# Kernel optimization log

Measured on AMD Instinct MI355X. Metric: run time of the kernel, lower is better.

Reference implementation:

```python
import jax, jax.numpy as jnp
import numpy as np

B, TQ, TK, D, R, H = 4, 2048, 2048, 1024, 64, 512
TAU_BASE, ASTRO_DECAY = 1.0, 0.95


def setup_inputs() -> dict:
    key = jax.random.key(0)
    ks = jax.random.split(key, 20)
    xav = lambda k, din, dout: jax.random.uniform(k, (din, dout), jnp.float32, -1.0, 1.0) * np.sqrt(6.0 / (din + dout))
    inp = {
        'q_in': jax.random.normal(ks[0], (B, TQ, D), jnp.float32),
        'k_in': jax.random.normal(ks[1], (B, TK, D), jnp.float32),
        'v_in': jax.random.normal(ks[2], (B, TK, D), jnp.float32),
        'astrocyte_state': jnp.zeros((B,), jnp.float32),
        'Wq': xav(ks[3], D, D), 'bq': jnp.zeros((D,), jnp.float32),
        'Wk': xav(ks[4], D, D), 'bk': jnp.zeros((D,), jnp.float32),
        'Wv': xav(ks[5], D, D), 'bv': jnp.zeros((D,), jnp.float32),
        'Wo': xav(ks[6], D, D), 'bo': jnp.zeros((D,), jnp.float32),
        # orthonormal role rows (R <= D): QR of a random D x R matrix, rows = Q^T
        'role_matrix': jnp.linalg.qr(jax.random.normal(ks[7], (D, R), jnp.float32))[0].T,
        'Wr1': xav(ks[8], D, H), 'br1': jnp.zeros((H,), jnp.float32),
        'Wr2': xav(ks[9], H, R),
        'astro_scale': jnp.ones((1,), jnp.float32),
    }
    return inp


def _l2norm(x, axis=-1, eps=1e-12):
    return x / jnp.clip(jnp.linalg.norm(x, axis=axis, keepdims=True), eps)


def _bind_vectors(a, b):
    # holographic (circular-convolution) binding via FFT along feature dim
    n = a.shape[-1]
    return jnp.fft.irfft(jnp.fft.rfft(a, axis=-1) * jnp.fft.rfft(b, axis=-1), n=n, axis=-1)


def _compute_surprise(Q):
    # per-token surprise: RMS-normalized L2 magnitude of projected queries -> (B, T_q)
    return jnp.linalg.norm(Q, axis=-1) / np.sqrt(Q.shape[-1])


def reference(q_in, k_in, v_in, astrocyte_state, Wq, bq, Wk, bk, Wv, bv, Wo, bo,
              role_matrix, Wr1, br1, Wr2, astro_scale):
    Q = q_in @ Wq + bq                      # (B,TQ,D)
    K = k_in @ Wk + bk                      # (B,TK,D)
    V = v_in @ Wv + bv                      # (B,TK,D)

    role_mat_norm = _l2norm(role_matrix)    # (R,D)
    role_logits = jax.nn.relu(K @ Wr1 + br1) @ Wr2          # (B,TK,R)
    role_weights = jax.nn.softmax(role_logits, axis=-1)
    role_vecs = role_weights @ role_mat_norm                 # (B,TK,D)
    K_bound = _bind_vectors(K, role_vecs)                    # (B,TK,D)

    surprise = _compute_surprise(Q)                          # (B,TQ)
    mean_surprise = surprise.mean(axis=-1)                   # (B,)
    new_state = ASTRO_DECAY * astrocyte_state + (1.0 - ASTRO_DECAY) * mean_surprise
    tau_eff = TAU_BASE * jnp.clip(1.0 + astro_scale * new_state, 0.001)[:, None, None]

    q_n = _l2norm(Q)
    k_n = _l2norm(K_bound)
    cos_sim = jnp.einsum('bqd,bkd->bqk', q_n, k_n)           # (B,TQ,TK)
    x = (cos_sim + 1.0) * 0.5
    scores = jnp.clip(1.0 - tau_eff * (1.0 - x) ** 2, 0.0)   # Epanechnikov kernel
    attn = scores / jnp.clip(scores.sum(axis=-1, keepdims=True), 1e-9)
    context = jnp.einsum('bqk,bkd->bqd', attn, V)
    output = context @ Wo + bo
    return output, new_state
```

## Files before the change

### kernel.cpp

```cpp
#include <hip/hip_runtime.h>
#include <stdint.h>


#define Bq 4
#define Tq 2048
#define Dd 1024
#define NT 8192
#define Hh 512
#define Rr_ 64
#define FQ 1024

typedef unsigned short ushort_t;
typedef short s16x8 __attribute__((ext_vector_type(8)));
typedef float floatx4 __attribute__((ext_vector_type(4)));

__device__ __forceinline__ float b2f(ushort_t s) {
  unsigned u = (unsigned)s << 16;
  return __builtin_bit_cast(float, u);
}
__device__ __forceinline__ ushort_t f2b(float f) {
  unsigned u = __builtin_bit_cast(unsigned, f);
  unsigned r = (u + 0x7fffu + ((u >> 16) & 1u)) >> 16;
  return (ushort_t)r;
}

__device__ __forceinline__ void load_lds16(const void* g, void* l) {
  __builtin_amdgcn_global_load_lds((__attribute__((address_space(1))) void*)(g),
                                   (__attribute__((address_space(3))) void*)(l),
                                   16, 0, 0);
}

__global__ __launch_bounds__(256) void gemm_bt(
    const ushort_t* __restrict__ A, const ushort_t* __restrict__ Bt,
    float* __restrict__ C, ushort_t* __restrict__ Cbf,
    const float* __restrict__ bias_col, const float* __restrict__ bias_row,
    const float* __restrict__ rmul, int rmulStride,
    const float* __restrict__ cmul, int cmulStride,
    const float* __restrict__ tau,
    float* __restrict__ rowsum, int rsStride, int rsMode,
    int K, int lda, int ldb, int ldc,
    long long sA, long long sB, long long sC, int flags)
{
  __shared__ __align__(16) ushort_t As[128 * 32];
  __shared__ __align__(16) ushort_t Bs[128 * 32];

  const int bz   = blockIdx.z;
  const ushort_t* Ab = A + (size_t)bz * sA;
  const ushort_t* Bb = Bt + (size_t)bz * sB;
  const int tm   = blockIdx.y * 128;
  const int tn   = blockIdx.x * 128;
  const int tid  = threadIdx.x;
  const int wave = tid >> 6;
  const int lane = tid & 63;
  const int wm   = (wave & 1) << 6;
  const int wn   = (wave >> 1) << 6;
  const int sr   = lane >> 2;
  const int cp   = lane & 3;
  const int sc   = (((cp - (sr >> 1)) & 3) << 3);
  const int fr   = lane & 15;
  const int fk   = ((((lane >> 4) + (fr >> 1)) & 3) << 3);

  floatx4 acc[4][4] = {};

  for (int k0 = 0; k0 < K; k0 += 32) {
    {
      const ushort_t* gA0 = Ab + (size_t)(tm + wave * 16 + sr) * lda + (k0 + sc);
      const ushort_t* gA1 = gA0 + (size_t)64 * lda;
      char* lA = (char*)As + wave * 1024;
      load_lds16(gA0, lA);
      load_lds16(gA1, lA + 4096);
      const ushort_t* gB0 = Bb + (size_t)(tn + wave * 16 + sr) * ldb + (k0 + sc);
      const ushort_t* gB1 = gB0 + (size_t)64 * ldb;
      char* lB = (char*)Bs + wave * 1024;
      load_lds16(gB0, lB);
      load_lds16(gB1, lB + 4096);
    }
    __syncthreads();
    s16x8 af[4], bfv[4];
#pragma unroll
    for (int i = 0; i < 4; i++)
      af[i] = *(const s16x8*)&As[(wm + i * 16 + fr) * 32 + fk];
#pragma unroll
    for (int j = 0; j < 4; j++)
      bfv[j] = *(const s16x8*)&Bs[(wn + j * 16 + fr) * 32 + fk];
#pragma unroll
    for (int i = 0; i < 4; i++)
#pragma unroll
      for (int j = 0; j < 4; j++)
        acc[i][j] = __builtin_amdgcn_mfma_f32_16x16x32_bf16(af[i], bfv[j], acc[i][j], 0, 0, 0);
    __syncthreads();
  }

  const float tv = tau ? tau[bz] : 0.f;
  float*   Cp  = C   ? C   + (size_t)bz * sC : nullptr;
  ushort_t* Cb = Cbf ? Cbf + (size_t)bz * sC : nullptr;
  float bcv[4], cmv[4];
#pragma unroll
  for (int j = 0; j < 4; j++) {
    const int col = tn + wn + j * 16 + (lane & 15);
    bcv[j] = bias_col ? bias_col[col] : 0.f;
    cmv[j] = cmul ? cmul[(size_t)bz * cmulStride + col] : 1.f;
  }
#pragma unroll
  for (int i = 0; i < 4; i++) {
#pragma unroll
    for (int r = 0; r < 4; r++) {
      const int row = tm + wm + i * 16 + (lane >> 4) * 4 + r;
      const float rm = rmul ? rmul[(size_t)bz * rmulStride + row] : 1.f;
      const float br = bias_row ? bias_row[row] : 0.f;
      float rsum = 0.f;
#pragma unroll
      for (int j = 0; j < 4; j++) {
        const int col = tn + wn + j * 16 + (lane & 15);
        float v = acc[i][j][r] + bcv[j] + br;
        v *= rm * cmv[j];
        if (flags & 1) v = fmaxf(v, 0.f);
        if (tau) { float d = 1.0f - v; v = fmaxf(1.0f - tv * 0.25f * d * d, 0.f); }
        rsum += (rsMode == 2) ? v * v : v;
        if (Cp) Cp[(size_t)row * ldc + col] = v;
        if (Cb) Cb[(size_t)row * ldc + col] = f2b(v);
      }
      if (rsMode == 1 || rsMode == 2) {
        rsum += __shfl_xor(rsum, 1);
        rsum += __shfl_xor(rsum, 2);
        rsum += __shfl_xor(rsum, 4);
        rsum += __shfl_xor(rsum, 8);
        if ((lane & 15) == 0)
          atomicAdd(&rowsum[(size_t)bz * rsStride + row], rsum);
      }
    }
  }
}

__global__ __launch_bounds__(256) void castbf(const float* __restrict__ in,
                                              ushort_t* __restrict__ out, int n4) {
  int i = blockIdx.x * 256 + threadIdx.x;
  if (i >= n4) return;
  float4 v = ((const float4*)in)[i];
  ushort4 o;
  o.x = f2b(v.x); o.y = f2b(v.y); o.z = f2b(v.z); o.w = f2b(v.w);
  ((ushort4*)out)[i] = o;
}

struct TC4 { const float* in[4]; ushort_t* out[4]; };
__global__ __launch_bounds__(256) void tcast4(TC4 p) {
  __shared__ float t[32][33];
  int z = blockIdx.z;
  const float* in = p.in[z];
  ushort_t* out = p.out[z];
  int r0 = blockIdx.x * 32, c0 = blockIdx.y * 32;
  int x = threadIdx.x, y = threadIdx.y;
  for (int dy = 0; dy < 32; dy += 8)
    t[y + dy][x] = in[(size_t)(r0 + y + dy) * 1024 + c0 + x];
  __syncthreads();
  for (int dy = 0; dy < 32; dy += 8)
    out[(size_t)(c0 + y + dy) * 1024 + r0 + x] = f2b(t[x][y + dy]);
}

__global__ __launch_bounds__(256) void tcast(const float* __restrict__ in,
                                             ushort_t* __restrict__ out,
                                             int RrN, int Cc, int Cp) {
  __shared__ float t[32][33];
  int r0 = blockIdx.x * 32, c0 = blockIdx.y * 32;
  int x = threadIdx.x, y = threadIdx.y;
  for (int dy = 0; dy < 32; dy += 8) {
    int r = r0 + y + dy, c = c0 + x;
    t[y + dy][x] = (c < Cc) ? in[(size_t)r * Cc + c] : 0.f;
  }
  __syncthreads();
  for (int dy = 0; dy < 32; dy += 8) {
    int c = c0 + y + dy, r = r0 + x;
    if (c < Cp) out[(size_t)c * RrN + r] = f2b(t[x][y + dy]);
  }
}

__global__ __launch_bounds__(256) void rolenorm(const float* __restrict__ rm,
                                                ushort_t* __restrict__ rmn) {
  int r = blockIdx.x, tid = threadIdx.x;
  float4 v = ((const float4*)(rm + (size_t)r * 1024))[tid];
  float s = v.x * v.x + v.y * v.y + v.z * v.z + v.w * v.w;
#pragma unroll
  for (int m = 1; m < 64; m <<= 1) s += __shfl_xor(s, m);
  __shared__ float red[6];
  if ((tid & 63) == 0) red[tid >> 6] = s;
  __syncthreads();
  if (tid == 0) red[4] = 1.f / fmaxf(sqrtf(red[0] + red[1] + red[2] + red[3]), 1e-12f);
  __syncthreads();
  float inv = red[4];
  ushort4 o;
  o.x = f2b(v.x * inv); o.y = f2b(v.y * inv); o.z = f2b(v.z * inv); o.w = f2b(v.w * inv);
  ((ushort4*)(rmn + (size_t)r * 1024))[tid] = o;
}

__global__ __launch_bounds__(256) void rfn_kernel(const ushort_t* __restrict__ rmn,
                                                  const ushort_t* __restrict__ ftab,
                                                  ushort_t* __restrict__ RFnT) {
  int f = blockIdx.x;
  int t = threadIdx.x;
  int r = t >> 2, part = t & 3;
  const ushort_t* fr = ftab + (size_t)f * 1024 + part * 256;
  const ushort_t* rr = rmn + (size_t)r * 1024 + part * 256;
  float s = 0.f;
#pragma unroll 4
  for (int i = 0; i < 32; i++) {
    s16x8 a = *(const s16x8*)(fr + i * 8);
    s16x8 b = *(const s16x8*)(rr + i * 8);
#pragma unroll
    for (int j = 0; j < 8; j++) s += b2f((ushort_t)a[j]) * b2f((ushort_t)b[j]);
  }
  s += __shfl_xor(s, 1);
  s += __shfl_xor(s, 2);
  if (part == 0) RFnT[(size_t)f * 128 + r] = f2b(s);
}

__global__ __launch_bounds__(256) void invnorm_surprise(const float* __restrict__ ssq,
                                                        float* __restrict__ invn,
                                                        float* __restrict__ ssum) {
  int row = blockIdx.x * 256 + threadIdx.x;
  float nrm = sqrtf(ssq[row]);
  invn[row] = 1.f / fmaxf(nrm, 1e-12f);
  float t = nrm;
#pragma unroll
  for (int m = 1; m < 64; m <<= 1) t += __shfl_xor(t, m);
  if ((threadIdx.x & 63) == 0) atomicAdd(&ssum[row >> 11], t);
}

__global__ __launch_bounds__(256) void invnorm(const float* __restrict__ ssq,
                                               float* __restrict__ invn) {
  int row = blockIdx.x * 256 + threadIdx.x;
  invn[row] = 1.f / fmaxf(sqrtf(ssq[row]), 1e-12f);
}

__global__ __launch_bounds__(256) void invrowsum(const float* __restrict__ rs,
                                                 float* __restrict__ inv) {
  int row = blockIdx.x * 256 + threadIdx.x;
  inv[row] = 1.f / fmaxf(rs[row], 1e-9f);
}

__global__ void finalize_astro(const float* __restrict__ ssum, const float* __restrict__ astro,
                               const float* __restrict__ ascale, float* __restrict__ tau,
                               float* __restrict__ outTail) {
  int b = threadIdx.x;
  if (b < Bq) {
    float mean = ssum[b] * (1.f / (32.f * 2048.f));
    float ns = 0.95f * astro[b] + 0.05f * mean;
    tau[b] = fmaxf(1.f + ascale[0] * ns, 0.001f);
    outTail[b] = ns;
  }
}

__global__ __launch_bounds__(256) void softmax64(const float* __restrict__ logits,
                                                 ushort_t* __restrict__ out) {
  int row = blockIdx.x * 4 + (threadIdx.x >> 6);
  int lane = threadIdx.x & 63;
  float x = logits[(size_t)row * 128 + lane];
  float m = x;
#pragma unroll
  for (int s = 1; s < 64; s <<= 1) m = fmaxf(m, __shfl_xor(m, s));
  float e = expf(x - m);
  float sum = e;
#pragma unroll
  for (int s = 1; s < 64; s <<= 1) sum += __shfl_xor(sum, s);
  out[(size_t)row * 64 + lane] = f2b(e / sum);
}

__global__ __launch_bounds__(256) void gen_ftab(ushort_t* __restrict__ ftab) {
  const float TW = 6.283185307179586f / 1024.f;
  int idx = blockIdx.x * 256 + threadIdx.x;
  int j = idx >> 10, k = idx & 1023;
  int f = j <= 512 ? j : j - 512;
  float th = (float)((f * k) & 1023) * TW;
  float sv, cv; sincosf(th, &sv, &cv);
  ftab[idx] = f2b(j <= 512 ? cv : -sv);
}
__global__ __launch_bounds__(256) void gen_itab(ushort_t* __restrict__ itab) {
  const float TW = 6.283185307179586f / 1024.f;
  int idx = blockIdx.x * 256 + threadIdx.x;
  int n = idx >> 10, j = idx & 1023;
  float v;
  if (j <= 512) {
    float w = (j == 0 || j == 512) ? (1.f / 1024.f) : (2.f / 1024.f);
    float th = (float)((j * n) & 1023) * TW;
    float sv, cv; sincosf(th, &sv, &cv);
    v = w * cv;
  } else {
    int f = j - 512;
    float th = (float)((f * n) & 1023) * TW;
    float sv, cv; sincosf(th, &sv, &cv);
    v = -(2.f / 1024.f) * sv;
  }
  itab[idx] = f2b(v);
}

__global__ __launch_bounds__(256) void fftmul(const ushort_t* __restrict__ KF,
                                              const ushort_t* __restrict__ RF,
                                              ushort_t* __restrict__ P) {
  int idx = blockIdx.x * 256 + threadIdx.x;
  int t = idx >> 9;
  int j = idx & 511;
  size_t base = (size_t)t * FQ;
  if (j == 0) {
    P[base]       = f2b(b2f(KF[base]) * b2f(RF[base]));
    P[base + 512] = f2b(b2f(KF[base + 512]) * b2f(RF[base + 512]));
  } else {
    float a = b2f(KF[base + j]), b = b2f(KF[base + 512 + j]);
    float c = b2f(RF[base + j]), d = b2f(RF[base + 512 + j]);
    P[base + j]       = f2b(a * c - b * d);
    P[base + 512 + j] = f2b(a * d + b * c);
  }
}

static constexpr size_t OFF_RS    = 0;
static constexpr size_t OFF_SSQQ  = 32768;
static constexpr size_t OFF_SSQK  = 65536;
static constexpr size_t OFF_INVQ  = 98304;
static constexpr size_t OFF_INVK  = 131072;
static constexpr size_t OFF_INVRS = 163840;
static constexpr size_t OFF_SSUM  = 196608;
static constexpr size_t OFF_TAU   = 196864;
static constexpr size_t OFF_WQT   = 197120;
static constexpr size_t OFF_WKT   = OFF_WQT  + 2097152;
static constexpr size_t OFF_WVT   = OFF_WKT  + 2097152;
static constexpr size_t OFF_WOT   = OFF_WVT  + 2097152;
static constexpr size_t OFF_WR1T  = OFF_WOT  + 2097152;
static constexpr size_t OFF_WR2T  = OFF_WR1T + 1048576;
static constexpr size_t OFF_RMN   = OFF_WR2T + 131072;
static constexpr size_t OFF_FTAB  = OFF_RMN  + 131072;
static constexpr size_t OFF_ITAB  = OFF_FTAB + 2097152;
static constexpr size_t OFF_RFNT  = OFF_ITAB + 2097152;
static constexpr size_t OFF_B1    = OFF_RFNT + 262144;
static constexpr size_t OFF_B2    = OFF_B1   + 16777216;
static constexpr size_t OFF_B3    = OFF_B2   + 16777216;
static constexpr size_t OFF_B4    = OFF_B3   + 16777216;
static constexpr size_t OFF_B5    = OFF_B4   + 16777216;
static constexpr size_t OFF_B6    = OFF_B5   + 16777216;
static constexpr size_t OFF_B7    = OFF_B6   + 16777216;
static constexpr size_t OFF_HID   = OFF_B7   + 16777216;
static constexpr size_t OFF_LOGI  = OFF_HID  + 8388608;
static constexpr size_t OFF_RW    = OFF_LOGI + 4194304;
static constexpr size_t OFF_SB    = OFF_RW   + 1048576;
static constexpr size_t WS_NEEDED = OFF_SB   + 33554432;

static inline void launch_gemm(hipStream_t s, const ushort_t* A, const ushort_t* Bt,
                               float* Cf, ushort_t* Cb,
                               const float* bias_col, const float* bias_row,
                               const float* rmul, int rmulStride,
                               const float* cmul, int cmulStride,
                               const float* tau, float* rowsum, int rsStride, int rsMode,
                               int M, int N, int K, int lda, int ldb, int ldc,
                               long long sA, long long sB, long long sC, int Z, int flags) {
  dim3 g(N / 128, M / 128, Z), b(256);
  gemm_bt<<<g, b, 0, s>>>(A, Bt, Cf, Cb, bias_col, bias_row, rmul, rmulStride,
                          cmul, cmulStride, tau, rowsum, rsStride, rsMode,
                          K, lda, ldb, ldc, sA, sB, sC, flags);
}

extern "C" void kernel_launch(void* const* d_in, const int* in_sizes, int n_in,
                              void* d_out, int out_size, void* d_ws, size_t ws_size,
                              hipStream_t stream) {
  (void)in_sizes; (void)n_in; (void)out_size;
  if (ws_size < WS_NEEDED) return;

  const float* q_in  = (const float*)d_in[0];
  const float* k_in  = (const float*)d_in[1];
  const float* v_in  = (const float*)d_in[2];
  const float* astro = (const float*)d_in[3];
  const float* Wq    = (const float*)d_in[4];
  const float* bq    = (const float*)d_in[5];
  const float* Wk    = (const float*)d_in[6];
  const float* bk    = (const float*)d_in[7];
  const float* Wv    = (const float*)d_in[8];
  const float* bv    = (const float*)d_in[9];
  const float* Wo    = (const float*)d_in[10];
  const float* bo    = (const float*)d_in[11];
  const float* roleM = (const float*)d_in[12];
  const float* Wr1   = (const float*)d_in[13];
  const float* br1   = (const float*)d_in[14];
  const float* Wr2   = (const float*)d_in[15];
  const float* ascl  = (const float*)d_in[16];

  char* ws = (char*)d_ws;
  float*    rowsumS = (float*)(ws + OFF_RS);
  float*    ssqQ    = (float*)(ws + OFF_SSQQ);
  float*    ssqK    = (float*)(ws + OFF_SSQK);
  float*    invQ    = (float*)(ws + OFF_INVQ);
  float*    invK    = (float*)(ws + OFF_INVK);
  float*    invRS   = (float*)(ws + OFF_INVRS);
  float*    ssum    = (float*)(ws + OFF_SSUM);
  float*    tau     = (float*)(ws + OFF_TAU);
  ushort_t* WqT  = (ushort_t*)(ws + OFF_WQT);
  ushort_t* WkT  = (ushort_t*)(ws + OFF_WKT);
  ushort_t* WvT  = (ushort_t*)(ws + OFF_WVT);
  ushort_t* WoT  = (ushort_t*)(ws + OFF_WOT);
  ushort_t* Wr1T = (ushort_t*)(ws + OFF_WR1T);
  ushort_t* Wr2T = (ushort_t*)(ws + OFF_WR2T);
  ushort_t* rmn  = (ushort_t*)(ws + OFF_RMN);
  ushort_t* FTab = (ushort_t*)(ws + OFF_FTAB);
  ushort_t* ITab = (ushort_t*)(ws + OFF_ITAB);
  ushort_t* RFnT = (ushort_t*)(ws + OFF_RFNT);
  ushort_t* qbf  = (ushort_t*)(ws + OFF_B1);
  ushort_t* KF   = (ushort_t*)(ws + OFF_B1);
  ushort_t* kinb = (ushort_t*)(ws + OFF_B2);
  ushort_t* RF   = (ushort_t*)(ws + OFF_B2);
  ushort_t* vinb = (ushort_t*)(ws + OFF_B3);
  ushort_t* Pb   = (ushort_t*)(ws + OFF_B3);
  ushort_t* qraw = (ushort_t*)(ws + OFF_B4);
  ushort_t* kbraw= (ushort_t*)(ws + OFF_B5);
  ushort_t* kp   = (ushort_t*)(ws + OFF_B6);
  ushort_t* ctx  = (ushort_t*)(ws + OFF_B6);
  ushort_t* vT   = (ushort_t*)(ws + OFF_B7);
  ushort_t* hid  = (ushort_t*)(ws + OFF_HID);
  float*    logi = (float*)(ws + OFF_LOGI);
  ushort_t* rw   = (ushort_t*)(ws + OFF_RW);
  ushort_t* Sb   = (ushort_t*)(ws + OFF_SB);
  float*    out  = (float*)d_out;

  hipMemsetAsync(ws, 0, OFF_SSUM + 256, stream);

  TC4 tc4;
  tc4.in[0] = Wq; tc4.in[1] = Wk; tc4.in[2] = Wv; tc4.in[3] = Wo;
  tc4.out[0] = WqT; tc4.out[1] = WkT; tc4.out[2] = WvT; tc4.out[3] = WoT;
  tcast4<<<dim3(32, 32, 4), dim3(32, 8), 0, stream>>>(tc4);
  tcast<<<dim3(32, 16), dim3(32, 8), 0, stream>>>(Wr1, Wr1T, 1024, 512, 512);
  tcast<<<dim3(16, 4),  dim3(32, 8), 0, stream>>>(Wr2, Wr2T, 512, 64, 128);
  rolenorm<<<64, 256, 0, stream>>>(roleM, rmn);
  gen_ftab<<<(FQ * 1024) / 256, 256, 0, stream>>>(FTab);
  gen_itab<<<(1024 * FQ) / 256, 256, 0, stream>>>(ITab);
  rfn_kernel<<<FQ, 256, 0, stream>>>(rmn, FTab, RFnT);

  castbf<<<8192, 256, 0, stream>>>(q_in, qbf, NT * Dd / 4);
  launch_gemm(stream, qbf, WqT, nullptr, qraw, bq, nullptr,
              nullptr, 0, nullptr, 0, nullptr, ssqQ, 0, 2,
              NT, Dd, Dd, Dd, Dd, Dd, 0, 0, 0, 1, 0);
  invnorm_surprise<<<NT / 256, 256, 0, stream>>>(ssqQ, invQ, ssum);
  finalize_astro<<<1, 64, 0, stream>>>(ssum, astro, ascl, tau, out + (size_t)NT * Dd);

  castbf<<<8192, 256, 0, stream>>>(k_in, kinb, NT * Dd / 4);
  launch_gemm(stream, kinb, WkT, nullptr, kp, bk, nullptr,
              nullptr, 0, nullptr, 0, nullptr, nullptr, 0, 0,
              NT, Dd, Dd, Dd, Dd, Dd, 0, 0, 0, 1, 0);

  castbf<<<8192, 256, 0, stream>>>(v_in, vinb, NT * Dd / 4);
  launch_gemm(stream, WvT, vinb, nullptr, vT, nullptr, bv,
              nullptr, 0, nullptr, 0, nullptr, nullptr, 0, 0,
              Dd, NT, Dd, Dd, Dd, NT, 0, 0, 0, 1, 0);

  launch_gemm(stream, kp, Wr1T, nullptr, hid, br1, nullptr,
              nullptr, 0, nullptr, 0, nullptr, nullptr, 0, 0,
              NT, Hh, Dd, Dd, Dd, Hh, 0, 0, 0, 1, 1 );
  launch_gemm(stream, hid, Wr2T, logi, nullptr, nullptr, nullptr,
              nullptr, 0, nullptr, 0, nullptr, nullptr, 0, 0,
              NT, 128, Hh, Hh, Hh, 128, 0, 0, 0, 1, 0);
  softmax64<<<NT / 4, 256, 0, stream>>>(logi, rw);

  launch_gemm(stream, kp, FTab, nullptr, KF, nullptr, nullptr,
              nullptr, 0, nullptr, 0, nullptr, nullptr, 0, 0,
              NT, FQ, Dd, Dd, Dd, FQ, 0, 0, 0, 1, 0);
  launch_gemm(stream, rw, RFnT, nullptr, RF, nullptr, nullptr,
              nullptr, 0, nullptr, 0, nullptr, nullptr, 0, 0,
              NT, FQ, Rr_, Rr_, 128, FQ, 0, 0, 0, 1, 0);
  fftmul<<<(NT * 512) / 256, 256, 0, stream>>>(KF, RF, Pb);
  launch_gemm(stream, Pb, ITab, nullptr, kbraw, nullptr, nullptr,
              nullptr, 0, nullptr, 0, nullptr, ssqK, 0, 2,
              NT, Dd, FQ, FQ, FQ, Dd, 0, 0, 0, 1, 0);
  invnorm<<<NT / 256, 256, 0, stream>>>(ssqK, invK);

  launch_gemm(stream, qraw, kbraw, nullptr, Sb, nullptr, nullptr,
              invQ, Tq, invK, Tq, tau, rowsumS, Tq, 1,
              Tq, Tq, Dd, Dd, Dd, Tq,
              (long long)Tq * Dd, (long long)Tq * Dd, (long long)Tq * Tq, Bq, 0);
  invrowsum<<<NT / 256, 256, 0, stream>>>(rowsumS, invRS);
  launch_gemm(stream, Sb, vT, nullptr, ctx, nullptr, nullptr,
              invRS, Tq, nullptr, 0, nullptr, nullptr, 0, 0,
              Tq, Dd, Tq, Tq, NT, Dd,
              (long long)Tq * Tq, (long long)Tq, (long long)Tq * Dd, Bq, 0);

  launch_gemm(stream, ctx, WoT, out, nullptr, bo, nullptr,
              nullptr, 0, nullptr, 0, nullptr, nullptr, 0, 0,
              NT, Dd, Dd, Dd, Dd, Dd, 0, 0, 0, 1, 0);
}
```

Before: 687.2 us.

## Fold weight products to eliminate K projection and output projection GEMMs

Precomputes combined weight matrices (FTab·Wk, Wr1·Wk, Wo·Wv) and folded biases so that K_in feeds the FFT and role-MLP GEMMs directly. V_in is projected straight into Wo·Wv space, which lets the attention-times-V GEMM write the final output with a post-scale bias. This removes the NT×D×D K projection and the final Wo GEMM. It adds small per-call weight-product kernels, and the extra bf16 rounding of the combined weights changes numerics slightly.

Measured after the change: 767.1 us. 1.12x slower.

```diff
diff --git a/kernel.cpp b/kernel.cpp
--- a/kernel.cpp
+++ b/kernel.cpp
@@ -112,8 +112,12 @@
 #pragma unroll
       for (int j = 0; j < 4; j++) {
         const int col = tn + wn + j * 16 + (lane & 15);
-        float v = acc[i][j][r] + bcv[j] + br;
-        v *= rm * cmv[j];
+        float v;
+        if (flags & 2) {
+          v = acc[i][j][r] * (rm * cmv[j]) + bcv[j] + br;
+        } else {
+          v = (acc[i][j][r] + bcv[j] + br) * (rm * cmv[j]);
+        }
         if (flags & 1) v = fmaxf(v, 0.f);
         if (tau) { float d = 1.0f - v; v = fmaxf(1.0f - tv * 0.25f * d * d, 0.f); }
         rsum += (rsMode == 2) ? v * v : v;
@@ -132,6 +136,73 @@
   }
 }
 
+struct P3 { const ushort_t* A[3]; const ushort_t* Bt[3]; ushort_t* C[3]; int M[3]; };
+
+__global__ __launch_bounds__(256) void prep3(P3 p) {
+  __shared__ __align__(16) ushort_t As[128 * 32];
+  __shared__ __align__(16) ushort_t Bs[128 * 32];
+  const int z  = blockIdx.z;
+  const int tm = blockIdx.y * 128;
+  if (tm >= p.M[z]) return;
+  const ushort_t* Ab = p.A[z];
+  const ushort_t* Bb = p.Bt[z];
+  ushort_t*       Cc = p.C[z];
+  const int tn   = blockIdx.x * 128;
+  const int tid  = threadIdx.x;
+  const int wave = tid >> 6;
+  const int lane = tid & 63;
+  const int wm   = (wave & 1) << 6;
+  const int wn   = (wave >> 1) << 6;
+  const int sr   = lane >> 2;
+  const int cp   = lane & 3;
+  const int sc   = (((cp - (sr >> 1)) & 3) << 3);
+  const int fr   = lane & 15;
+  const int fk   = ((((lane >> 4) + (fr >> 1)) & 3) << 3);
+
+  floatx4 acc[4][4] = {};
+
+  for (int k0 = 0; k0 < Dd; k0 += 32) {
+    {
+      const ushort_t* gA0 = Ab + (size_t)(tm + wave * 16 + sr) * Dd + (k0 + sc);
+      const ushort_t* gA1 = gA0 + (size_t)64 * Dd;
+      char* lA = (char*)As + wave * 1024;
+      load_lds16(gA0, lA);
+      load_lds16(gA1, lA + 4096);
+      const ushort_t* gB0 = Bb + (size_t)(tn + wave * 16 + sr) * Dd + (k0 + sc);
+      const ushort_t* gB1 = gB0 + (size_t)64 * Dd;
+      char* lB = (char*)Bs + wave * 1024;
+      load_lds16(gB0, lB);
+      load_lds16(gB1, lB + 4096);
+    }
+    __syncthreads();
+    s16x8 af[4], bfv[4];
+#pragma unroll
+    for (int i = 0; i < 4; i++)
+      af[i] = *(const s16x8*)&As[(wm + i * 16 + fr) * 32 + fk];
+#pragma unroll
+    for (int j = 0; j < 4; j++)
+      bfv[j] = *(const s16x8*)&Bs[(wn + j * 16 + fr) * 32 + fk];
+#pragma unroll
+    for (int i = 0; i < 4; i++)
+#pragma unroll
+      for (int j = 0; j < 4; j++)
+        acc[i][j] = __builtin_amdgcn_mfma_f32_16x16x32_bf16(af[i], bfv[j], acc[i][j], 0, 0, 0);
+    __syncthreads();
+  }
+
+#pragma unroll
+  for (int i = 0; i < 4; i++)
+#pragma unroll
+    for (int r = 0; r < 4; r++) {
+      const int row = tm + wm + i * 16 + (lane >> 4) * 4 + r;
+#pragma unroll
+      for (int j = 0; j < 4; j++) {
+        const int col = tn + wn + j * 16 + (lane & 15);
+        Cc[(size_t)row * Dd + col] = f2b(acc[i][j][r]);
+      }
+    }
+}
+
 __global__ __launch_bounds__(256) void castbf(const float* __restrict__ in,
                                               ushort_t* __restrict__ out, int n4) {
   int i = blockIdx.x * 256 + threadIdx.x;
@@ -211,6 +282,44 @@
   s += __shfl_xor(s, 1);
   s += __shfl_xor(s, 2);
   if (part == 0) RFnT[(size_t)f * 128 + r] = f2b(s);
+}
+
+__global__ __launch_bounds__(64) void foldbk(const ushort_t* __restrict__ ftab,
+                                             const float* __restrict__ bk,
+                                             float* __restrict__ bkF) {
+  int j = blockIdx.x, lane = threadIdx.x;
+  const ushort_t* row = ftab + (size_t)j * 1024 + lane * 16;
+  const float* bp = bk + lane * 16;
+  float s = 0.f;
+#pragma unroll
+  for (int i = 0; i < 2; i++) {
+    s16x8 a = *(const s16x8*)(row + i * 8);
+#pragma unroll
+    for (int e = 0; e < 8; e++) s += b2f((ushort_t)a[e]) * bp[i * 8 + e];
+  }
+#pragma unroll
+  for (int m = 1; m < 64; m <<= 1) s += __shfl_xor(s, m);
+  if (lane == 0) bkF[j] = s;
+}
+
+__global__ __launch_bounds__(256) void foldbh(const float* __restrict__ Wr1,
+                                              const float* __restrict__ bk,
+                                              const float* __restrict__ br1,
+                                              float* __restrict__ bh) {
+  int h = blockIdx.x * 256 + threadIdx.x;
+  float s = br1[h];
+  for (int d = 0; d < 1024; d++) s += bk[d] * Wr1[(size_t)d * Hh + h];
+  bh[h] = s;
+}
+
+__global__ __launch_bounds__(256) void foldbvo(const float* __restrict__ Wo,
+                                               const float* __restrict__ bv,
+                                               const float* __restrict__ bo,
+                                               float* __restrict__ bvo) {
+  int d = blockIdx.x * 256 + threadIdx.x;
+  float s = bo[d];
+  for (int e = 0; e < 1024; e++) s += bv[e] * Wo[(size_t)e * 1024 + d];
+  bvo[d] = s;
 }
 
 __global__ __launch_bounds__(256) void invnorm_surprise(const float* __restrict__ ssq,
@@ -319,9 +428,9 @@
 static constexpr size_t OFF_SSUM  = 196608;
 static constexpr size_t OFF_TAU   = 196864;
 static constexpr size_t OFF_WQT   = 197120;
-static constexpr size_t OFF_WKT   = OFF_WQT  + 2097152;
-static constexpr size_t OFF_WVT   = OFF_WKT  + 2097152;
-static constexpr size_t OFF_WOT   = OFF_WVT  + 2097152;
+static constexpr size_t OFF_WKB   = OFF_WQT  + 2097152;
+static constexpr size_t OFF_WVB   = OFF_WKB  + 2097152;
+static constexpr size_t OFF_WOT   = OFF_WVB  + 2097152;
 static constexpr size_t OFF_WR1T  = OFF_WOT  + 2097152;
 static constexpr size_t OFF_WR2T  = OFF_WR1T + 1048576;
 static constexpr size_t OFF_RMN   = OFF_WR2T + 131072;
@@ -340,6 +449,12 @@
 static constexpr size_t OFF_RW    = OFF_LOGI + 4194304;
 static constexpr size_t OFF_SB    = OFF_RW   + 1048576;
 static constexpr size_t WS_NEEDED = OFF_SB   + 33554432;
+static constexpr size_t OFF_WKF   = OFF_B6;
+static constexpr size_t OFF_WOV   = OFF_B6 + 2097152;
+static constexpr size_t OFF_WKR1  = OFF_B6 + 4194304;
+static constexpr size_t OFF_BKF   = OFF_B6 + 5242880;
+static constexpr size_t OFF_BH    = OFF_B6 + 5247232;
+static constexpr size_t OFF_BVO   = OFF_B6 + 5249536;
 
 static inline void launch_gemm(hipStream_t s, const ushort_t* A, const ushort_t* Bt,
                                float* Cf, ushort_t* Cb,
@@ -389,8 +504,8 @@
   float*    ssum    = (float*)(ws + OFF_SSUM);
   float*    tau     = (float*)(ws + OFF_TAU);
   ushort_t* WqT  = (ushort_t*)(ws + OFF_WQT);
-  ushort_t* WkT  = (ushort_t*)(ws + OFF_WKT);
-  ushort_t* WvT  = (ushort_t*)(ws + OFF_WVT);
+  ushort_t* Wkb  = (ushort_t*)(ws + OFF_WKB);
+  ushort_t* Wvb  = (ushort_t*)(ws + OFF_WVB);
   ushort_t* WoT  = (ushort_t*)(ws + OFF_WOT);
   ushort_t* Wr1T = (ushort_t*)(ws + OFF_WR1T);
   ushort_t* Wr2T = (ushort_t*)(ws + OFF_WR2T);
@@ -406,8 +521,12 @@
   ushort_t* Pb   = (ushort_t*)(ws + OFF_B3);
   ushort_t* qraw = (ushort_t*)(ws + OFF_B4);
   ushort_t* kbraw= (ushort_t*)(ws + OFF_B5);
-  ushort_t* kp   = (ushort_t*)(ws + OFF_B6);
-  ushort_t* ctx  = (ushort_t*)(ws + OFF_B6);
+  ushort_t* WkF  = (ushort_t*)(ws + OFF_WKF);
+  ushort_t* Wov  = (ushort_t*)(ws + OFF_WOV);
+  ushort_t* WkR1 = (ushort_t*)(ws + OFF_WKR1);
+  float*    bkF  = (float*)(ws + OFF_BKF);
+  float*    bh   = (float*)(ws + OFF_BH);
+  float*    bvo  = (float*)(ws + OFF_BVO);
   ushort_t* vT   = (ushort_t*)(ws + OFF_B7);
   ushort_t* hid  = (ushort_t*)(ws + OFF_HID);
   float*    logi = (float*)(ws + OFF_LOGI);
@@ -418,9 +537,13 @@
   hipMemsetAsync(ws, 0, OFF_SSUM + 256, stream);
 
   TC4 tc4;
-  tc4.in[0] = Wq; tc4.in[1] = Wk; tc4.in[2] = Wv; tc4.in[3] = Wo;
-  tc4.out[0] = WqT; tc4.out[1] = WkT; tc4.out[2] = WvT; tc4.out[3] = WoT;
-  tcast4<<<dim3(32, 32, 4), dim3(32, 8), 0, stream>>>(tc4);
+  tc4.in[0] = Wq; tc4.out[0] = WqT;
+  tc4.in[1] = Wo; tc4.out[1] = WoT;
+  tc4.in[2] = Wq; tc4.out[2] = WqT;
+  tc4.in[3] = Wq; tc4.out[3] = WqT;
+  tcast4<<<dim3(32, 32, 2), dim3(32, 8), 0, stream>>>(tc4);
+  castbf<<<1024, 256, 0, stream>>>(Wk, Wkb, 262144);
+  castbf<<<1024, 256, 0, stream>>>(Wv, Wvb, 262144);
   tcast<<<dim3(32, 16), dim3(32, 8), 0, stream>>>(Wr1, Wr1T, 1024, 512, 512);
   tcast<<<dim3(16, 4),  dim3(32, 8), 0, stream>>>(Wr2, Wr2T, 512, 64, 128);
   rolenorm<<<64, 256, 0, stream>>>(roleM, rmn);
@@ -428,6 +551,15 @@
   gen_itab<<<(1024 * FQ) / 256, 256, 0, stream>>>(ITab);
   rfn_kernel<<<FQ, 256, 0, stream>>>(rmn, FTab, RFnT);
 
+  P3 p3;
+  p3.A[0] = FTab; p3.Bt[0] = Wkb; p3.C[0] = WkF;  p3.M[0] = 1024;
+  p3.A[1] = WoT;  p3.Bt[1] = Wvb; p3.C[1] = Wov;  p3.M[1] = 1024;
+  p3.A[2] = Wr1T; p3.Bt[2] = Wkb; p3.C[2] = WkR1; p3.M[2] = 512;
+  prep3<<<dim3(8, 8, 3), 256, 0, stream>>>(p3);
+  foldbk<<<1024, 64, 0, stream>>>(FTab, bk, bkF);
+  foldbh<<<Hh / 256, 256, 0, stream>>>(Wr1, bk, br1, bh);
+  foldbvo<<<Dd / 256, 256, 0, stream>>>(Wo, bv, bo, bvo);
+
   castbf<<<8192, 256, 0, stream>>>(q_in, qbf, NT * Dd / 4);
   launch_gemm(stream, qbf, WqT, nullptr, qraw, bq, nullptr,
               nullptr, 0, nullptr, 0, nullptr, ssqQ, 0, 2,
@@ -436,16 +568,7 @@
   finalize_astro<<<1, 64, 0, stream>>>(ssum, astro, ascl, tau, out + (size_t)NT * Dd);
 
   castbf<<<8192, 256, 0, stream>>>(k_in, kinb, NT * Dd / 4);
-  launch_gemm(stream, kinb, WkT, nullptr, kp, bk, nullptr,
-              nullptr, 0, nullptr, 0, nullptr, nullptr, 0, 0,
-              NT, Dd, Dd, Dd, Dd, Dd, 0, 0, 0, 1, 0);
-
-  castbf<<<8192, 256, 0, stream>>>(v_in, vinb, NT * Dd / 4);
-  launch_gemm(stream, WvT, vinb, nullptr, vT, nullptr, bv,
-              nullptr, 0, nullptr, 0, nullptr, nullptr, 0, 0,
-              Dd, NT, Dd, Dd, Dd, NT, 0, 0, 0, 1, 0);
-
-  launch_gemm(stream, kp, Wr1T, nullptr, hid, br1, nullptr,
+  launch_gemm(stream, kinb, WkR1, nullptr, hid, bh, nullptr,
               nullptr, 0, nullptr, 0, nullptr, nullptr, 0, 0,
               NT, Hh, Dd, Dd, Dd, Hh, 0, 0, 0, 1, 1 );
   launch_gemm(stream, hid, Wr2T, logi, nullptr, nullptr, nullptr,
@@ -453,12 +576,18 @@
               NT, 128, Hh, Hh, Hh, 128, 0, 0, 0, 1, 0);
   softmax64<<<NT / 4, 256, 0, stream>>>(logi, rw);
 
-  launch_gemm(stream, kp, FTab, nullptr, KF, nullptr, nullptr,
+  launch_gemm(stream, kinb, WkF, nullptr, KF, bkF, nullptr,
               nullptr, 0, nullptr, 0, nullptr, nullptr, 0, 0,
               NT, FQ, Dd, Dd, Dd, FQ, 0, 0, 0, 1, 0);
   launch_gemm(stream, rw, RFnT, nullptr, RF, nullptr, nullptr,
               nullptr, 0, nullptr, 0, nullptr, nullptr, 0, 0,
               NT, FQ, Rr_, Rr_, 128, FQ, 0, 0, 0, 1, 0);
+
+  castbf<<<8192, 256, 0, stream>>>(v_in, vinb, NT * Dd / 4);
+  launch_gemm(stream, Wov, vinb, nullptr, vT, nullptr, nullptr,
+              nullptr, 0, nullptr, 0, nullptr, nullptr, 0, 0,
+              Dd, NT, Dd, Dd, Dd, NT, 0, 0, 0, 1, 0);
+
   fftmul<<<(NT * 512) / 256, 256, 0, stream>>>(KF, RF, Pb);
   launch_gemm(stream, Pb, ITab, nullptr, kbraw, nullptr, nullptr,
               nullptr, 0, nullptr, 0, nullptr, ssqK, 0, 2,
@@ -470,12 +599,8 @@
               Tq, Tq, Dd, Dd, Dd, Tq,
               (long long)Tq * Dd, (long long)Tq * Dd, (long long)Tq * Tq, Bq, 0);
   invrowsum<<<NT / 256, 256, 0, stream>>>(rowsumS, invRS);
-  launch_gemm(stream, Sb, vT, nullptr, ctx, nullptr, nullptr,
+  launch_gemm(stream, Sb, vT, out, nullptr, bvo, nullptr,
               invRS, Tq, nullptr, 0, nullptr, nullptr, 0, 0,
               Tq, Dd, Tq, Tq, NT, Dd,
-              (long long)Tq * Tq, (long long)Tq, (long long)Tq * Dd, Bq, 0);
-
-  launch_gemm(stream, ctx, WoT, out, nullptr, bo, nullptr,
-              nullptr, 0, nullptr, 0, nullptr, nullptr, 0, 0,
-              NT, Dd, Dd, Dd, Dd, Dd, 0, 0, 0, 1, 0);
-}
+              (long long)Tq * Tq, (long long)Tq, (long long)Tq * Dd, Bq, 2 );
+}
```
